# Kernel tuning notes

Measured on AMD Instinct MI355X. Metric: run time of the kernel, lower is better.

Reference implementation:

```python
import jax, jax.numpy as jnp
import numpy as np

E, T, IN, OUT = 8, 16384, 1024, 1024  # n_groups, total_tokens, in_features, out_features


def setup_inputs() -> dict:
    key = jax.random.key(0)
    kx, kw, ks = jax.random.split(key, 3)
    x = jax.random.normal(kx, (T, IN), dtype=jnp.float32)
    # kaiming_uniform-ish scale for weight [E, OUT, IN]
    weight = jax.random.normal(kw, (E, OUT, IN), dtype=jnp.float32) * (1.0 / np.sqrt(IN))
    # ragged segment lengths that sum exactly to T (random cut points)
    cuts = jnp.sort(jax.random.randint(ks, (E - 1,), 0, T + 1)).astype(jnp.int32)
    seg_lens = jnp.diff(
        jnp.concatenate([jnp.zeros((1,), jnp.int32), cuts, jnp.full((1,), T, jnp.int32)])
    )
    return {"x": x, "weight": weight, "seg_lens": seg_lens}


def reference(x, weight, seg_lens):
    # Grouped GEMM: row t of x is multiplied by weight[g(t)].T where g(t) is the
    # segment (expert) that token t falls into per seg_lens. trans_b=True.
    n_groups = weight.shape[0]
    bounds = jnp.cumsum(seg_lens)                                  # [E]
    seg_id = jnp.searchsorted(bounds, jnp.arange(x.shape[0]), side="right")  # [T]
    y = jnp.zeros((x.shape[0], weight.shape[1]), dtype=x.dtype)
    for e in range(n_groups):  # small fixed loop over groups
        y = y + jnp.where((seg_id == e)[:, None], x @ weight[e].T, 0)
    return y
```

## Files before the change

kernel.cpp:

```cpp
#include <hip/hip_runtime.h>

#define T_TOK  16384
#define IN_F   1024
#define OUT_F  1024
#define NE     8

typedef __bf16 bf16;
typedef bf16  bf16x4 __attribute__((ext_vector_type(4)));
typedef bf16  bf16x8 __attribute__((ext_vector_type(8)));
typedef float f32x4  __attribute__((ext_vector_type(4)));

#define CVT_THREADS 256
#define NX_CHUNKS (T_TOK * IN_F / 4)
#define NW_CHUNKS (NE * OUT_F * IN_F / 4)
#define NO_CHUNKS (T_TOK * OUT_F / 4)
#define NCVT_CHUNKS (NX_CHUNKS + NW_CHUNKS)
#define NALL_CHUNKS (NCVT_CHUNKS + NO_CHUNKS)

__global__ __launch_bounds__(CVT_THREADS)
void cvt_and_zero(const float* __restrict__ x, const float* __restrict__ w,
                  bf16* __restrict__ xb, bf16* __restrict__ wb,
                  float* __restrict__ out)
{
    for (int i = blockIdx.x * CVT_THREADS + threadIdx.x; i < NALL_CHUNKS;
         i += gridDim.x * CVT_THREADS) {
        if (i < NCVT_CHUNKS) {
            const bool isx = (i < NX_CHUNKS);
            const int  j   = isx ? i : i - NX_CHUNKS;
            f32x4 v = isx ? ((const f32x4*)x)[j] : ((const f32x4*)w)[j];
            bf16x4 h;
            #pragma unroll
            for (int k = 0; k < 4; ++k) h[k] = (bf16)v[k];
            if (isx) ((bf16x4*)xb)[j] = h;
            else     ((bf16x4*)wb)[j] = h;
        } else {
            f32x4 z = {0.f, 0.f, 0.f, 0.f};
            ((f32x4*)out)[i - NCVT_CHUNKS] = z;
        }
    }
}

#define BM 256
#define BN 256
#define BK 64
#define GTHREADS 512
#define NBLOCKS 256
#define KCH (IN_F / BK)

__device__ __forceinline__ void gld_lds16(const bf16* g, bf16* l) {
    __builtin_amdgcn_global_load_lds(
        (const __attribute__((address_space(1))) void*)g,
        (__attribute__((address_space(3))) void*)l,
        16, 0, 0);
}

__device__ __forceinline__ void resolve_slot(const int* sl, int slot,
                                             int& e_sel, int& row0, int& rows)
{
    e_sel = -1; row0 = 0; rows = 0;
    int start = 0, acct = 0;
    #pragma unroll
    for (int e = 0; e < NE; ++e) {
        int len = sl[e];
        int nt  = (len + BM - 1) >> 8;
        if (e_sel < 0 && slot >= acct && slot < acct + nt) {
            e_sel = e;
            row0  = start + (slot - acct) * BM;
            int rm = start + len - row0;
            rows = rm < BM ? rm : BM;
        }
        acct  += nt;
        start += len;
    }
}

__global__ __launch_bounds__(GTHREADS)
void grouped_gemm_hybrid(const bf16* __restrict__ xb,
                         const bf16* __restrict__ wb,
                         const int*  __restrict__ seg_lens,
                         float* __restrict__ out)
{
    __shared__ __align__(16) bf16 As[2][BM * BK];
    __shared__ __align__(16) bf16 Bs[2][BN * BK];

    const int tid  = threadIdx.x;
    const int lane = tid & 63;
    const int wave = tid >> 6;
    const int wr   = wave >> 2;
    const int wc   = wave & 3;
    const int quad = lane >> 4;
    const int l16  = lane & 15;
    const int rq   = lane >> 3;
    const int ke   = (lane & 7) * 8;
    const int q0   = wave * 4;
    const int b    = blockIdx.x;

    int sl[NE];
    #pragma unroll
    for (int e = 0; e < NE; ++e) sl[e] = seg_lens[e];

    int n_slots = 0;
    #pragma unroll
    for (int e = 0; e < NE; ++e) n_slots += (sl[e] + BM - 1) >> 8;
    const int L = n_slots * (OUT_F / BN);

    if (b < L) {
        const int slot = b >> 2;
        const int col0 = (b & 3) << 8;
        int e_sel, row0, rows;
        resolve_slot(sl, slot, e_sel, row0, rows);

        const bf16* wbase = wb + ((size_t)e_sel * OUT_F + (size_t)col0) * IN_F;

        const bf16* ga[4];
        const bf16* gb[4];
        #pragma unroll
        for (int i = 0; i < 4; ++i) {
            int q  = wave * 4 + i;
            int ra = row0 + q * 8 + rq;
            if (ra > T_TOK - 1) ra = T_TOK - 1;
            ga[i] = xb + (size_t)ra * IN_F + ke;
            gb[i] = wbase + (size_t)(q * 8 + rq) * IN_F + ke;
        }

        f32x4 acc[8][4] = {};

        #pragma unroll
        for (int i = 0; i < 4; ++i) {
            gld_lds16(ga[i], &As[0][(q0 + i) * 512]);
            gld_lds16(gb[i], &Bs[0][(q0 + i) * 512]);
        }
        __syncthreads();

        int cur = 0;
        #pragma unroll
        for (int ks = 0; ks < KCH; ++ks) {
            const int kn = (ks + 1) * BK;
            if (ks + 1 < KCH) {
                #pragma unroll
                for (int i = 0; i < 4; ++i) {
                    gld_lds16(ga[i] + kn, &As[cur ^ 1][(q0 + i) * 512]);
                    gld_lds16(gb[i] + kn, &Bs[cur ^ 1][(q0 + i) * 512]);
                }
            }

            #pragma unroll
            for (int kk = 0; kk < 2; ++kk) {
                bf16x8 af[8], bfr[4];
                #pragma unroll
                for (int t = 0; t < 8; ++t)
                    af[t] = *(const bf16x8*)(
                        &As[cur][(wr * 128 + t * 16 + l16) * BK + kk * 32 + quad * 8]);
                #pragma unroll
                for (int v = 0; v < 4; ++v)
                    bfr[v] = *(const bf16x8*)(
                        &Bs[cur][(wc * 64 + v * 16 + l16) * BK + kk * 32 + quad * 8]);
                #pragma unroll
                for (int t = 0; t < 8; ++t)
                    #pragma unroll
                    for (int v = 0; v < 4; ++v)
                        acc[t][v] = __builtin_amdgcn_mfma_f32_16x16x32_bf16(
                            af[t], bfr[v], acc[t][v], 0, 0, 0);
            }

            __syncthreads();
            cur ^= 1;
        }

        #pragma unroll
        for (int t = 0; t < 8; ++t) {
            #pragma unroll
            for (int r = 0; r < 4; ++r) {
                int row = wr * 128 + t * 16 + quad * 4 + r;
                if (row < rows) {
                    size_t ob = (size_t)(row0 + row) * OUT_F + col0 + wc * 64;
                    #pragma unroll
                    for (int v = 0; v < 4; ++v)
                        out[ob + v * 16 + l16] = acc[t][v][r];
                }
            }
        }
    }

    const int Uleft = (L - NBLOCKS) * KCH;
    if (Uleft <= 0) return;
    {
        const int base = Uleft >> 8;
        const int rem  = Uleft & 255;
        int u    = NBLOCKS * KCH + b * base + (b < rem ? b : rem);
        int uend = u + base + (b < rem ? 1 : 0);

        while (u < uend) {
            const int tile = u >> 4;
            const int kc0  = u & (KCH - 1);
            int kc1 = kc0 + (uend - u);
            if (kc1 > KCH) kc1 = KCH;
            u += kc1 - kc0;

            const int slot = tile >> 2;
            const int col0 = (tile & 3) << 8;
            int e_sel, row0, rows;
            resolve_slot(sl, slot, e_sel, row0, rows);

            const bf16* wbase = wb + ((size_t)e_sel * OUT_F + (size_t)col0) * IN_F;

            const bf16* ga[4];
            const bf16* gb[4];
            #pragma unroll
            for (int i = 0; i < 4; ++i) {
                int q  = wave * 4 + i;
                int ra = row0 + q * 8 + rq;
                if (ra > T_TOK - 1) ra = T_TOK - 1;
                ga[i] = xb + (size_t)ra * IN_F + ke;
                gb[i] = wbase + (size_t)(q * 8 + rq) * IN_F + ke;
            }

            f32x4 acc[8][4] = {};

            {
                const int kb = kc0 * BK;
                #pragma unroll
                for (int i = 0; i < 4; ++i) {
                    gld_lds16(ga[i] + kb, &As[0][(q0 + i) * 512]);
                    gld_lds16(gb[i] + kb, &Bs[0][(q0 + i) * 512]);
                }
            }
            __syncthreads();

            int cur = 0;
            for (int ks = kc0; ks < kc1; ++ks) {
                const int kn = (ks + 1) * BK;
                if (ks + 1 < kc1) {
                    #pragma unroll
                    for (int i = 0; i < 4; ++i) {
                        gld_lds16(ga[i] + kn, &As[cur ^ 1][(q0 + i) * 512]);
                        gld_lds16(gb[i] + kn, &Bs[cur ^ 1][(q0 + i) * 512]);
                    }
                }

                #pragma unroll
                for (int kk = 0; kk < 2; ++kk) {
                    bf16x8 af[8], bfr[4];
                    #pragma unroll
                    for (int t = 0; t < 8; ++t)
                        af[t] = *(const bf16x8*)(
                            &As[cur][(wr * 128 + t * 16 + l16) * BK + kk * 32 + quad * 8]);
                    #pragma unroll
                    for (int v = 0; v < 4; ++v)
                        bfr[v] = *(const bf16x8*)(
                            &Bs[cur][(wc * 64 + v * 16 + l16) * BK + kk * 32 + quad * 8]);
                    #pragma unroll
                    for (int t = 0; t < 8; ++t)
                        #pragma unroll
                        for (int v = 0; v < 4; ++v)
                            acc[t][v] = __builtin_amdgcn_mfma_f32_16x16x32_bf16(
                                af[t], bfr[v], acc[t][v], 0, 0, 0);
                }

                __syncthreads();
                cur ^= 1;
            }

            #pragma unroll
            for (int t = 0; t < 8; ++t) {
                #pragma unroll
                for (int r = 0; r < 4; ++r) {
                    int row = wr * 128 + t * 16 + quad * 4 + r;
                    if (row < rows) {
                        size_t ob = (size_t)(row0 + row) * OUT_F + col0 + wc * 64;
                        #pragma unroll
                        for (int v = 0; v < 4; ++v)
                            unsafeAtomicAdd(&out[ob + v * 16 + l16], acc[t][v][r]);
                    }
                }
            }
        }
    }
}

#define FBM 128
#define FBK 32
#define FTHREADS 256
#define FROW_SLOTS 136

__global__ __launch_bounds__(FTHREADS)
void grouped_gemm_f32io_bf16(const float* __restrict__ x,
                             const float* __restrict__ wgt,
                             const int*  __restrict__ seg_lens,
                             float* __restrict__ out)
{
    __shared__ __align__(16) bf16 Asf[FBM * FBK];
    __shared__ __align__(16) bf16 Bsf[FBM * FBK];

    const int m    = blockIdx.y;
    const int col0 = blockIdx.x * FBM;

    int e_sel = -1, row0 = 0, rows = 0;
    {
        int start = 0, acct = 0;
        #pragma unroll
        for (int e = 0; e < NE; ++e) {
            int len = seg_lens[e];
            int nt  = (len + FBM - 1) >> 7;
            if (e_sel < 0 && m >= acct && m < acct + nt) {
                e_sel = e;
                row0  = start + (m - acct) * FBM;
                int rem = start + len - row0;
                rows = rem < FBM ? rem : FBM;
            }
            acct  += nt;
            start += len;
        }
    }
    if (e_sel < 0) return;

    const int tid  = threadIdx.x;
    const int lane = tid & 63;
    const int wave = tid >> 6;
    const int wm   = (wave >> 1) * 64;
    const int wn   = (wave & 1) * 64;
    const int quad = lane >> 4;
    const int l16  = lane & 15;

    const float* wbase = wgt + ((size_t)e_sel * OUT_F + (size_t)col0) * IN_F;

    f32x4 acc[4][4] = {};

    for (int k0 = 0; k0 < IN_F; k0 += FBK) {
        f32x4 a_st[4], b_st[4];
        #pragma unroll
        for (int t = 0; t < 4; ++t) {
            int c  = t * FTHREADS + tid;
            int rg = row0 + (c >> 3);
            if (rg > T_TOK - 1) rg = T_TOK - 1;
            a_st[t] = *(const f32x4*)(x + (size_t)rg * IN_F + k0 + (c & 7) * 4);
            b_st[t] = *(const f32x4*)(wbase + (size_t)(c >> 3) * IN_F + k0 + (c & 7) * 4);
        }

        __syncthreads();

        #pragma unroll
        for (int t = 0; t < 4; ++t) {
            int c = t * FTHREADS + tid;
            bf16x4 ha, hb;
            #pragma unroll
            for (int j = 0; j < 4; ++j) { ha[j] = (bf16)a_st[t][j]; hb[j] = (bf16)b_st[t][j]; }
            *(bf16x4*)(&Asf[(c >> 3) * FBK + (c & 7) * 4]) = ha;
            *(bf16x4*)(&Bsf[(c >> 3) * FBK + (c & 7) * 4]) = hb;
        }
        __syncthreads();

        bf16x8 af[4], bfr[4];
        #pragma unroll
        for (int t = 0; t < 4; ++t)
            af[t] = *(const bf16x8*)(&Asf[(wm + t * 16 + l16) * FBK + quad * 8]);
        #pragma unroll
        for (int v = 0; v < 4; ++v)
            bfr[v] = *(const bf16x8*)(&Bsf[(wn + v * 16 + l16) * FBK + quad * 8]);

        #pragma unroll
        for (int t = 0; t < 4; ++t)
            #pragma unroll
            for (int v = 0; v < 4; ++v)
                acc[t][v] = __builtin_amdgcn_mfma_f32_16x16x32_bf16(
                    af[t], bfr[v], acc[t][v], 0, 0, 0);
    }

    #pragma unroll
    for (int t = 0; t < 4; ++t) {
        #pragma unroll
        for (int r = 0; r < 4; ++r) {
            int row = wm + t * 16 + quad * 4 + r;
            if (row < rows) {
                size_t ob = (size_t)(row0 + row) * OUT_F + col0;
                #pragma unroll
                for (int v = 0; v < 4; ++v)
                    out[ob + wn + v * 16 + l16] = acc[t][v][r];
            }
        }
    }
}

extern "C" void kernel_launch(void* const* d_in, const int* in_sizes, int n_in,
                              void* d_out, int out_size, void* d_ws, size_t ws_size,
                              hipStream_t stream) {
    const float* x   = (const float*)d_in[0];
    const float* wgt = (const float*)d_in[1];
    const int*   seg = (const int*)d_in[2];
    float* out = (float*)d_out;

    const size_t xbytes = (size_t)T_TOK * IN_F * sizeof(bf16);
    const size_t wbytes = (size_t)NE * OUT_F * IN_F * sizeof(bf16);

    if (ws_size >= xbytes + wbytes) {
        bf16* xb = (bf16*)d_ws;
        bf16* wb = (bf16*)((char*)d_ws + xbytes);
        cvt_and_zero<<<dim3(2048, 1, 1), dim3(CVT_THREADS, 1, 1), 0, stream>>>(
            x, wgt, xb, wb, out);
        grouped_gemm_hybrid<<<dim3(NBLOCKS, 1, 1), dim3(GTHREADS, 1, 1), 0, stream>>>(
            xb, wb, seg, out);
    } else {
        grouped_gemm_f32io_bf16<<<dim3(OUT_F / FBM, FROW_SLOTS, 1),
                                  dim3(FTHREADS, 1, 1), 0, stream>>>(x, wgt, seg, out);
    }
}
```

Baseline: 224.8 us.

## Split hybrid grouped GEMM into separate main and split-K surplus kernels

The single hybrid kernel, which did full tiles and then split-K surplus work with atomics, is split into two kernels launched back to back. Each kernel now carries only one code path, which should lower register pressure and code size per kernel and drop the main-loop full unroll. The cost is an extra kernel launch and the loss of overlap between the tail of the main tiles and the start of the surplus work.

Measured after the change: 236.8 us. +5.3%, slower.

```diff
diff --git a/kernel.cpp b/kernel.cpp
--- a/kernel.cpp
+++ b/kernel.cpp
@@ -75,10 +75,113 @@
 }
 
 __global__ __launch_bounds__(GTHREADS)
-void grouped_gemm_hybrid(const bf16* __restrict__ xb,
-                         const bf16* __restrict__ wb,
-                         const int*  __restrict__ seg_lens,
-                         float* __restrict__ out)
+void grouped_gemm_main(const bf16* __restrict__ xb,
+                       const bf16* __restrict__ wb,
+                       const int*  __restrict__ seg_lens,
+                       float* __restrict__ out)
+{
+    __shared__ __align__(16) bf16 As[2][BM * BK];
+    __shared__ __align__(16) bf16 Bs[2][BN * BK];
+
+    const int tile = blockIdx.x;
+    const int slot = tile >> 2;
+    const int col0 = (tile & 3) << 8;
+
+    int sl[NE];
+    #pragma unroll
+    for (int e = 0; e < NE; ++e) sl[e] = seg_lens[e];
+
+    int e_sel, row0, rows;
+    resolve_slot(sl, slot, e_sel, row0, rows);
+    if (e_sel < 0) return;
+
+    const int tid  = threadIdx.x;
+    const int lane = tid & 63;
+    const int wave = tid >> 6;
+    const int wr   = wave >> 2;
+    const int wc   = wave & 3;
+    const int quad = lane >> 4;
+    const int l16  = lane & 15;
+    const int rq   = lane >> 3;
+    const int ke   = (lane & 7) * 8;
+    const int q0   = wave * 4;
+
+    const bf16* wbase = wb + ((size_t)e_sel * OUT_F + (size_t)col0) * IN_F;
+
+    const bf16* ga[4];
+    const bf16* gb[4];
+    #pragma unroll
+    for (int i = 0; i < 4; ++i) {
+        int q  = wave * 4 + i;
+        int ra = row0 + q * 8 + rq;
+        if (ra > T_TOK - 1) ra = T_TOK - 1;
+        ga[i] = xb + (size_t)ra * IN_F + ke;
+        gb[i] = wbase + (size_t)(q * 8 + rq) * IN_F + ke;
+    }
+
+    f32x4 acc[8][4] = {};
+
+    #pragma unroll
+    for (int i = 0; i < 4; ++i) {
+        gld_lds16(ga[i], &As[0][(q0 + i) * 512]);
+        gld_lds16(gb[i], &Bs[0][(q0 + i) * 512]);
+    }
+    __syncthreads();
+
+    int cur = 0;
+    for (int ks = 0; ks < KCH; ++ks) {
+        const int kn = (ks + 1) * BK;
+        if (kn < IN_F) {
+            #pragma unroll
+            for (int i = 0; i < 4; ++i) {
+                gld_lds16(ga[i] + kn, &As[cur ^ 1][(q0 + i) * 512]);
+                gld_lds16(gb[i] + kn, &Bs[cur ^ 1][(q0 + i) * 512]);
+            }
+        }
+
+        #pragma unroll
+        for (int kk = 0; kk < 2; ++kk) {
+            bf16x8 af[8], bfr[4];
+            #pragma unroll
+            for (int t = 0; t < 8; ++t)
+                af[t] = *(const bf16x8*)(
+                    &As[cur][(wr * 128 + t * 16 + l16) * BK + kk * 32 + quad * 8]);
+            #pragma unroll
+            for (int v = 0; v < 4; ++v)
+                bfr[v] = *(const bf16x8*)(
+                    &Bs[cur][(wc * 64 + v * 16 + l16) * BK + kk * 32 + quad * 8]);
+            #pragma unroll
+            for (int t = 0; t < 8; ++t)
+                #pragma unroll
+                for (int v = 0; v < 4; ++v)
+                    acc[t][v] = __builtin_amdgcn_mfma_f32_16x16x32_bf16(
+                        af[t], bfr[v], acc[t][v], 0, 0, 0);
+        }
+
+        __syncthreads();
+        cur ^= 1;
+    }
+
+    #pragma unroll
+    for (int t = 0; t < 8; ++t) {
+        #pragma unroll
+        for (int r = 0; r < 4; ++r) {
+            int row = wr * 128 + t * 16 + quad * 4 + r;
+            if (row < rows) {
+                size_t ob = (size_t)(row0 + row) * OUT_F + col0 + wc * 64;
+                #pragma unroll
+                for (int v = 0; v < 4; ++v)
+                    out[ob + v * 16 + l16] = acc[t][v][r];
+            }
+        }
+    }
+}
+
+__global__ __launch_bounds__(GTHREADS)
+void grouped_gemm_surplus(const bf16* __restrict__ xb,
+                          const bf16* __restrict__ wb,
+                          const int*  __restrict__ seg_lens,
+                          float* __restrict__ out)
 {
     __shared__ __align__(16) bf16 As[2][BM * BK];
     __shared__ __align__(16) bf16 Bs[2][BN * BK];
@@ -104,9 +207,23 @@
     for (int e = 0; e < NE; ++e) n_slots += (sl[e] + BM - 1) >> 8;
     const int L = n_slots * (OUT_F / BN);
 
-    if (b < L) {
-        const int slot = b >> 2;
-        const int col0 = (b & 3) << 8;
+    const int Uleft = (L - NBLOCKS) * KCH;
+    if (Uleft <= 0) return;
+
+    const int base = Uleft >> 8;
+    const int rem  = Uleft & 255;
+    int u    = NBLOCKS * KCH + b * base + (b < rem ? b : rem);
+    int uend = u + base + (b < rem ? 1 : 0);
+
+    while (u < uend) {
+        const int tile = u >> 4;
+        const int kc0  = u & (KCH - 1);
+        int kc1 = kc0 + (uend - u);
+        if (kc1 > KCH) kc1 = KCH;
+        u += kc1 - kc0;
+
+        const int slot = tile >> 2;
+        const int col0 = (tile & 3) << 8;
         int e_sel, row0, rows;
         resolve_slot(sl, slot, e_sel, row0, rows);
 
@@ -125,18 +242,20 @@
 
         f32x4 acc[8][4] = {};
 
-        #pragma unroll
-        for (int i = 0; i < 4; ++i) {
-            gld_lds16(ga[i], &As[0][(q0 + i) * 512]);
-            gld_lds16(gb[i], &Bs[0][(q0 + i) * 512]);
+        {
+            const int kb = kc0 * BK;
+            #pragma unroll
+            for (int i = 0; i < 4; ++i) {
+                gld_lds16(ga[i] + kb, &As[0][(q0 + i) * 512]);
+                gld_lds16(gb[i] + kb, &Bs[0][(q0 + i) * 512]);
+            }
         }
         __syncthreads();
 
         int cur = 0;
-        #pragma unroll
-        for (int ks = 0; ks < KCH; ++ks) {
+        for (int ks = kc0; ks < kc1; ++ks) {
             const int kn = (ks + 1) * BK;
-            if (ks + 1 < KCH) {
+            if (ks + 1 < kc1) {
                 #pragma unroll
                 for (int i = 0; i < 4; ++i) {
                     gld_lds16(ga[i] + kn, &As[cur ^ 1][(q0 + i) * 512]);
@@ -176,102 +295,7 @@
                     size_t ob = (size_t)(row0 + row) * OUT_F + col0 + wc * 64;
                     #pragma unroll
                     for (int v = 0; v < 4; ++v)
-                        out[ob + v * 16 + l16] = acc[t][v][r];
-                }
-            }
-        }
-    }
-
-    const int Uleft = (L - NBLOCKS) * KCH;
-    if (Uleft <= 0) return;
-    {
-        const int base = Uleft >> 8;
-        const int rem  = Uleft & 255;
-        int u    = NBLOCKS * KCH + b * base + (b < rem ? b : rem);
-        int uend = u + base + (b < rem ? 1 : 0);
-
-        while (u < uend) {
-            const int tile = u >> 4;
-            const int kc0  = u & (KCH - 1);
-            int kc1 = kc0 + (uend - u);
-            if (kc1 > KCH) kc1 = KCH;
-            u += kc1 - kc0;
-
-            const int slot = tile >> 2;
-            const int col0 = (tile & 3) << 8;
-            int e_sel, row0, rows;
-            resolve_slot(sl, slot, e_sel, row0, rows);
-
-            const bf16* wbase = wb + ((size_t)e_sel * OUT_F + (size_t)col0) * IN_F;
-
-            const bf16* ga[4];
-            const bf16* gb[4];
-            #pragma unroll
-            for (int i = 0; i < 4; ++i) {
-                int q  = wave * 4 + i;
-                int ra = row0 + q * 8 + rq;
-                if (ra > T_TOK - 1) ra = T_TOK - 1;
-                ga[i] = xb + (size_t)ra * IN_F + ke;
-                gb[i] = wbase + (size_t)(q * 8 + rq) * IN_F + ke;
-            }
-
-            f32x4 acc[8][4] = {};
-
-            {
-                const int kb = kc0 * BK;
-                #pragma unroll
-                for (int i = 0; i < 4; ++i) {
-                    gld_lds16(ga[i] + kb, &As[0][(q0 + i) * 512]);
-                    gld_lds16(gb[i] + kb, &Bs[0][(q0 + i) * 512]);
-                }
-            }
-            __syncthreads();
-
-            int cur = 0;
-            for (int ks = kc0; ks < kc1; ++ks) {
-                const int kn = (ks + 1) * BK;
-                if (ks + 1 < kc1) {
-                    #pragma unroll
-                    for (int i = 0; i < 4; ++i) {
-                        gld_lds16(ga[i] + kn, &As[cur ^ 1][(q0 + i) * 512]);
-                        gld_lds16(gb[i] + kn, &Bs[cur ^ 1][(q0 + i) * 512]);
-                    }
-                }
-
-                #pragma unroll
-                for (int kk = 0; kk < 2; ++kk) {
-                    bf16x8 af[8], bfr[4];
-                    #pragma unroll
-                    for (int t = 0; t < 8; ++t)
-                        af[t] = *(const bf16x8*)(
-                            &As[cur][(wr * 128 + t * 16 + l16) * BK + kk * 32 + quad * 8]);
-                    #pragma unroll
-                    for (int v = 0; v < 4; ++v)
-                        bfr[v] = *(const bf16x8*)(
-                            &Bs[cur][(wc * 64 + v * 16 + l16) * BK + kk * 32 + quad * 8]);
-                    #pragma unroll
-                    for (int t = 0; t < 8; ++t)
-                        #pragma unroll
-                        for (int v = 0; v < 4; ++v)
-                            acc[t][v] = __builtin_amdgcn_mfma_f32_16x16x32_bf16(
-                                af[t], bfr[v], acc[t][v], 0, 0, 0);
-                }
-
-                __syncthreads();
-                cur ^= 1;
-            }
-
-            #pragma unroll
-            for (int t = 0; t < 8; ++t) {
-                #pragma unroll
-                for (int r = 0; r < 4; ++r) {
-                    int row = wr * 128 + t * 16 + quad * 4 + r;
-                    if (row < rows) {
-                        size_t ob = (size_t)(row0 + row) * OUT_F + col0 + wc * 64;
-                        #pragma unroll
-                        for (int v = 0; v < 4; ++v)
-                            unsafeAtomicAdd(&out[ob + v * 16 + l16], acc[t][v][r]);
-                    }
+                        unsafeAtomicAdd(&out[ob + v * 16 + l16], acc[t][v][r]);
                 }
             }
         }
@@ -397,7 +421,9 @@
         bf16* wb = (bf16*)((char*)d_ws + xbytes);
         cvt_and_zero<<<dim3(2048, 1, 1), dim3(CVT_THREADS, 1, 1), 0, stream>>>(
             x, wgt, xb, wb, out);
-        grouped_gemm_hybrid<<<dim3(NBLOCKS, 1, 1), dim3(GTHREADS, 1, 1), 0, stream>>>(
+        grouped_gemm_main<<<dim3(NBLOCKS, 1, 1), dim3(GTHREADS, 1, 1), 0, stream>>>(
+            xb, wb, seg, out);
+        grouped_gemm_surplus<<<dim3(NBLOCKS, 1, 1), dim3(GTHREADS, 1, 1), 0, stream>>>(
             xb, wb, seg, out);
     } else {
         grouped_gemm_f32io_bf16<<<dim3(OUT_F / FBM, FROW_SLOTS, 1),
```
